# Kernel optimization log

Measured on AMD Instinct MI355X. Metric: run time of the kernel, lower is better.

The kernel has to match this reference:

```python
import jax, jax.numpy as jnp
import numpy as np

B, T, NH, HD = 2, 2048, 12, 128
HIDDEN = NH * HD
EPS = 1.1920928955078125e-07  # torch fp32 finfo eps (F.rms_norm default)


def _rope_cos_sin(T, d_half, base=10000.0):
    inv = 1.0 / (base ** (jnp.arange(d_half, dtype=jnp.float32) / d_half))
    t = jnp.arange(T, dtype=jnp.float32)
    f = t[:, None] * inv[None, :]  # [T, d_half]
    return jnp.cos(f)[None, :, None, :], jnp.sin(f)[None, :, None, :]


def apply_rotary_emb(x, cos, sin):
    d = x.shape[3] // 2
    x1, x2 = x[..., :d], x[..., d:]
    return jnp.concatenate([x1 * cos + x2 * sin, x1 * -sin + x2 * cos], axis=3)


def rms_norm(x):
    return x * jax.lax.rsqrt(jnp.mean(x * x, axis=-1, keepdims=True) + EPS)


def setup_inputs() -> dict:
    key = jax.random.key(0)
    ks = jax.random.split(key, 5)
    x = jax.random.normal(ks[0], (B, T, HIDDEN), dtype=jnp.float32)
    cos, sin = _rope_cos_sin(T, HD // 2)
    s = 1.0 / np.sqrt(HIDDEN)
    Wq = jax.random.normal(ks[1], (HIDDEN, HIDDEN), dtype=jnp.float32) * s
    Wk = jax.random.normal(ks[2], (HIDDEN, HIDDEN), dtype=jnp.float32) * s
    Wv = jax.random.normal(ks[3], (HIDDEN, HIDDEN), dtype=jnp.float32) * s
    Wp = jax.random.normal(ks[4], (HIDDEN, HIDDEN), dtype=jnp.float32) * s
    return {"x": x, "cos": cos, "sin": sin, "Wq": Wq, "Wk": Wk, "Wv": Wv,
            "Wp": Wp, "window": 1024}


def reference(x, cos, sin, Wq, Wk, Wv, Wp, window):
    Bx, Tx, _ = x.shape
    q = (x @ Wq.T).reshape(Bx, Tx, NH, HD)
    k = (x @ Wk.T).reshape(Bx, Tx, NH, HD)
    v = (x @ Wv.T).reshape(Bx, Tx, NH, HD)
    q = rms_norm(apply_rotary_emb(q, cos, sin))
    k = rms_norm(apply_rotary_emb(k, cos, sin))
    # causal + sliding-window attention (dense, matching the sdpa fallback)
    scale = 1.0 / np.sqrt(HD)
    scores = jnp.einsum('bqhd,bkhd->bhqk', q, k) * scale
    row = jnp.arange(Tx)[:, None]
    col = jnp.arange(Tx)[None, :]
    mask = (col <= row) & (row - col <= window)
    scores = jnp.where(mask[None, None], scores, jnp.finfo(scores.dtype).min)
    attn = jax.nn.softmax(scores, axis=-1)
    y = jnp.einsum('bhqk,bkhd->bqhd', attn, v).reshape(Bx, Tx, HIDDEN)
    return y @ Wp.T
```

## Files before the change

kernel.cpp:

```cpp
#include <hip/hip_runtime.h>
#include <stdint.h>

#define HIDDEN 1536
#define NHEAD 12
#define HD 128
#define TSEQ 2048
#define NROWS 4096
#define KDIM HIDDEN
#define EPS_F 1.1920928955078125e-07f
#define SCALE_LOG2E 0.12751879110195655f
#define FIXSUB 16.6f

typedef unsigned short u16;
typedef __bf16 bf16x8_t __attribute__((ext_vector_type(8)));
typedef float f32x4_t __attribute__((ext_vector_type(4)));

#define MFMA16(a, b, c) __builtin_amdgcn_mfma_f32_16x16x32_bf16((a), (b), (c), 0, 0, 0)
#define GLL(srcp, dstp) \
  __builtin_amdgcn_global_load_lds((const __attribute__((address_space(1))) void*)(srcp), \
                                   (__attribute__((address_space(3))) void*)(dstp), 16, 0, 0)

__device__ __forceinline__ u16 f2bf(float f) {
  unsigned u = __builtin_bit_cast(unsigned, f);
  u = (u + 0x7fffu + ((u >> 16) & 1u)) >> 16;
  return (u16)u;
}
__device__ __forceinline__ float bfu(u16 v) {
  return __builtin_bit_cast(float, ((unsigned)v) << 16);
}

__global__ __launch_bounds__(256) void cast_kernel(const float* __restrict__ in,
                                                   u16* __restrict__ out, int n) {
  int i = (blockIdx.x * 256 + threadIdx.x) * 4;
  if (i >= n) return;
  float4 v = *reinterpret_cast<const float4*>(in + i);
  uint2 pk;
  pk.x = (unsigned)f2bf(v.x) | ((unsigned)f2bf(v.y) << 16);
  pk.y = (unsigned)f2bf(v.z) | ((unsigned)f2bf(v.w) << 16);
  *reinterpret_cast<uint2*>(out + i) = pk;
}

__global__ __launch_bounds__(256) void cast4_kernel(
    const float* __restrict__ a, const float* __restrict__ b, const float* __restrict__ c,
    const float* __restrict__ d, u16* __restrict__ oa, u16* __restrict__ ob,
    u16* __restrict__ oc, u16* __restrict__ od, int n) {
  const float* in;
  u16* out;
  switch (blockIdx.y) {
    case 0: in = a; out = oa; break;
    case 1: in = b; out = ob; break;
    case 2: in = c; out = oc; break;
    default: in = d; out = od; break;
  }
  int i = (blockIdx.x * 256 + threadIdx.x) * 4;
  if (i >= n) return;
  float4 v = *reinterpret_cast<const float4*>(in + i);
  uint2 pk;
  pk.x = (unsigned)f2bf(v.x) | ((unsigned)f2bf(v.y) << 16);
  pk.y = (unsigned)f2bf(v.z) | ((unsigned)f2bf(v.w) << 16);
  *reinterpret_cast<uint2*>(out + i) = pk;
}

__device__ __forceinline__ void gemm_mainloop64(const u16* __restrict__ A,
                                                const u16* __restrict__ W, int M0, int N0,
                                                u16* lds, f32x4_t acc[4][4], int tid) {
  const int w = tid >> 6, l = tid & 63;
  const int lrow = l & 15, kg = l >> 4;
  const int wr = (w >> 1) * 64, wc = (w & 1) * 64;
  const int row0 = tid >> 3, j0 = tid & 7;
  const unsigned jsw = (unsigned)((j0 ^ (row0 & 7)) * 8);
  unsigned offA = (unsigned)((M0 + row0) * KDIM) + jsw;
  unsigned offW = (unsigned)((N0 + row0) * KDIM) + jsw;
  const u16* A1 = A + 32 * KDIM; const u16* A2 = A + 64 * KDIM; const u16* A3 = A + 96 * KDIM;
  const u16* W1 = W + 32 * KDIM; const u16* W2 = W + 64 * KDIM; const u16* W3 = W + 96 * KDIM;
  auto issue = [&](int buf) {
    u16* da = lds + buf * 8192 + w * 512;
    u16* dw = lds + 16384 + buf * 8192 + w * 512;
    GLL(A + offA, da);          GLL(A1 + offA, da + 2048);
    GLL(A2 + offA, da + 4096);  GLL(A3 + offA, da + 6144);
    GLL(W + offW, dw);          GLL(W1 + offW, dw + 2048);
    GLL(W2 + offW, dw + 4096);  GLL(W3 + offW, dw + 6144);
    offA += 64; offW += 64;
  };
  issue(0);
  const int NT = KDIM / 64;
#pragma unroll 1
  for (int kt = 0; kt < NT; ++kt) {
    const int cur = kt & 1;
    if (kt + 1 < NT) {
      issue(cur ^ 1);
      asm volatile("s_waitcnt vmcnt(8)" ::: "memory");
    } else {
      asm volatile("s_waitcnt vmcnt(0)" ::: "memory");
    }
    __builtin_amdgcn_s_barrier();
    asm volatile("" ::: "memory");
    const u16* Ab = lds + cur * 8192;
    const u16* Wb = lds + 16384 + cur * 8192;
#pragma unroll
    for (int s = 0; s < 2; ++s) {
      bf16x8_t af[4], bf_[4];
#pragma unroll
      for (int mi = 0; mi < 4; ++mi) {
        const int row = wr + mi * 16 + lrow;
        af[mi] = *reinterpret_cast<const bf16x8_t*>(Ab + row * 64 +
                                                    (((s << 2) | kg) ^ (row & 7)) * 8);
      }
#pragma unroll
      for (int ni = 0; ni < 4; ++ni) {
        const int row = wc + ni * 16 + lrow;
        bf_[ni] = *reinterpret_cast<const bf16x8_t*>(Wb + row * 64 +
                                                     (((s << 2) | kg) ^ (row & 7)) * 8);
      }
#pragma unroll
      for (int mi = 0; mi < 4; ++mi)
#pragma unroll
        for (int ni = 0; ni < 4; ++ni)
          acc[mi][ni] = MFMA16(af[mi], bf_[ni], acc[mi][ni]);
    }
    asm volatile("s_waitcnt lgkmcnt(0)" ::: "memory");
    __builtin_amdgcn_s_barrier();
    asm volatile("" ::: "memory");
  }
}

__global__ __launch_bounds__(256) void gemm_qkv_kernel(
    const u16* __restrict__ xb, const u16* __restrict__ wq, const u16* __restrict__ wk,
    const u16* __restrict__ wv, const float* __restrict__ cosp, const float* __restrict__ sinp,
    u16* __restrict__ qh, u16* __restrict__ kh, u16* __restrict__ vt) {
  __shared__ __align__(16) u16 lds[32768];
  const int tid = threadIdx.x;
  const int wgid = blockIdx.x;
  const int xcd = wgid & 7, c = wgid >> 3;
  const int m = ((xcd & 3) << 3) + (c & 7);
  const int nz = ((xcd >> 2) * 18) + (c >> 3);
  const int z = nz / 12, n = nz % 12;
  const int M0 = m * 128, N0 = n * 128;
  const u16* W = (z == 0) ? wq : (z == 1) ? wk : wv;
  f32x4_t acc[4][4] = {};
  gemm_mainloop64(xb, W, M0, N0, lds, acc, tid);
  const int w = tid >> 6, l = tid & 63;
  const int lrow = l & 15, kg = l >> 4;
  const int wr = (w >> 1) * 64, wc = (w & 1) * 64;
  char* cs = reinterpret_cast<char*>(lds);
  if (z == 2) {
#pragma unroll
    for (int mi = 0; mi < 4; ++mi)
#pragma unroll
      for (int ni = 0; ni < 4; ++ni)
#pragma unroll
        for (int r = 0; r < 4; ++r) {
          const int t_l = wr + mi * 16 + kg * 4 + r;
          const int d = wc + ni * 16 + lrow;
          const int bofs = (d * 256 + t_l * 2) ^ ((d & 7) << 4);
          *reinterpret_cast<u16*>(cs + bofs) = f2bf(acc[mi][ni][r]);
        }
  } else {
#pragma unroll
    for (int mi = 0; mi < 4; ++mi)
#pragma unroll
      for (int ni = 0; ni < 4; ++ni)
#pragma unroll
        for (int r = 0; r < 4; ++r) {
          const int t_l = wr + mi * 16 + kg * 4 + r;
          const int d = wc + ni * 16 + lrow;
          const int bofs = (t_l * 256 + d * 2) ^ ((t_l & 7) << 4);
          *reinterpret_cast<u16*>(cs + bofs) = f2bf(acc[mi][ni][r]);
        }
  }
  __syncthreads();
  const int rr = tid >> 1, hh = tid & 1;
  const int bb = M0 >> 11;
  const int t0 = M0 & (TSEQ - 1);
  const size_t bhn = (size_t)(bb * NHEAD + n);
  if (z == 2) {
    u16* dst = vt + (bhn * HD + rr) * TSEQ + t0 + hh * 64;
    const char* base = cs + rr * 256 + hh * 128;
#pragma unroll
    for (int j = 0; j < 8; ++j) {
      uint4 v = *reinterpret_cast<const uint4*>(base + ((j ^ (rr & 7)) * 16));
      *reinterpret_cast<uint4*>(dst + j * 8) = v;
    }
  } else {
    const int t = t0 + rr;
    const float* cosb = cosp + t * 64;
    const float* sinb = sinp + t * 64;
    const char* base = cs + rr * 256;
    float ss = 0.0f;
    unsigned pk[32];
#pragma unroll
    for (int j = 0; j < 8; ++j) {
      const int jp = (j ^ (rr & 7)) * 16;
      uint4 vo = *reinterpret_cast<const uint4*>(base + hh * 128 + jp);
      uint4 vx = *reinterpret_cast<const uint4*>(base + (hh ^ 1) * 128 + jp);
      const unsigned vo32[4] = {vo.x, vo.y, vo.z, vo.w};
      const unsigned vx32[4] = {vx.x, vx.y, vx.z, vx.w};
      const float* cj = cosb + j * 8;
      const float* sj = sinb + j * 8;
#pragma unroll
      for (int q2 = 0; q2 < 4; ++q2) {
        float o0 = bfu((u16)(vo32[q2] & 0xffffu)), o1 = bfu((u16)(vo32[q2] >> 16));
        float x0 = bfu((u16)(vx32[q2] & 0xffffu)), x1 = bfu((u16)(vx32[q2] >> 16));
        float cc0 = cj[q2 * 2], cc1 = cj[q2 * 2 + 1];
        float s0 = sj[q2 * 2], s1 = sj[q2 * 2 + 1];
        float y0 = hh ? __builtin_fmaf(o0, cc0, -x0 * s0) : __builtin_fmaf(o0, cc0, x0 * s0);
        float y1 = hh ? __builtin_fmaf(o1, cc1, -x1 * s1) : __builtin_fmaf(o1, cc1, x1 * s1);
        ss = __builtin_fmaf(y0, y0, __builtin_fmaf(y1, y1, ss));
        pk[j * 4 + q2] = (unsigned)f2bf(y0) | ((unsigned)f2bf(y1) << 16);
      }
    }
    ss += __shfl_xor(ss, 1, 64);
    const float rinv = rsqrtf(ss * (1.0f / 128.0f) + EPS_F);
    u16* dst = ((z == 0) ? qh : kh) + (bhn * TSEQ + t) * HD + hh * 64;
#pragma unroll
    for (int j = 0; j < 8; ++j) {
      unsigned o[4];
#pragma unroll
      for (int q2 = 0; q2 < 4; ++q2) {
        float y0 = bfu((u16)(pk[j * 4 + q2] & 0xffffu)) * rinv;
        float y1 = bfu((u16)(pk[j * 4 + q2] >> 16)) * rinv;
        o[q2] = (unsigned)f2bf(y0) | ((unsigned)f2bf(y1) << 16);
      }
      uint4 v;
      v.x = o[0]; v.y = o[1]; v.z = o[2]; v.w = o[3];
      *reinterpret_cast<uint4*>(dst + j * 8) = v;
    }
  }
}

__global__ __launch_bounds__(256) void gemm_out_kernel(const u16* __restrict__ yh,
                                                       const u16* __restrict__ wp,
                                                       float* __restrict__ out) {
  __shared__ __align__(16) u16 lds[32768];
  const int tid = threadIdx.x;
  const int wgid = blockIdx.x;
  const int xcd = wgid & 7, c = wgid >> 3;
  const int m = ((xcd & 3) << 3) + (c & 7);
  const int n = ((xcd >> 2) * 6) + (c >> 3);
  const int M0 = m * 128, N0 = n * 128;
  f32x4_t acc[4][4] = {};
  gemm_mainloop64(yh, wp, M0, N0, lds, acc, tid);
  const int w = tid >> 6, l = tid & 63;
  const int lrow = l & 15, kg = l >> 4;
  const int wr = (w >> 1) * 64, wc = (w & 1) * 64;
#pragma unroll
  for (int mi = 0; mi < 4; ++mi)
#pragma unroll
    for (int ni = 0; ni < 4; ++ni)
#pragma unroll
      for (int r = 0; r < 4; ++r) {
        const int grow = M0 + wr + mi * 16 + kg * 4 + r;
        const int gcol = N0 + wc + ni * 16 + lrow;
        out[(size_t)grow * HIDDEN + gcol] = acc[mi][ni][r];
      }
}

__global__ __launch_bounds__(512, 4) void attn_kernel(const u16* __restrict__ qh,
                                                      const u16* __restrict__ kh,
                                                      const u16* __restrict__ vt,
                                                      u16* __restrict__ yh,
                                                      const int* __restrict__ winp) {
  __shared__ __align__(16) u16 Kl[2][8192];
  __shared__ __align__(16) u16 Vl[8192];
  __shared__ __align__(16) u16 Pl[8][1024];
  const int tid = threadIdx.x, w = tid >> 6, l = tid & 63;
  const int lrow = l & 15, kg = l >> 4;
  const int bid = blockIdx.x;
  const int swz = (bid & 7) * 48 + (bid >> 3);
  const int qb = swz & 15;
  const int bh = swz >> 4;
  const int h = bh % NHEAD, b = bh / NHEAD;
  const int win = winp[0];
  const u16* Q = qh + (size_t)bh * TSEQ * HD;
  const u16* K = kh + (size_t)bh * TSEQ * HD;
  const u16* V = vt + (size_t)bh * HD * TSEQ;
  const int qw = qb * 128 + w * 16;
  bf16x8_t aq[4];
#pragma unroll
  for (int ks = 0; ks < 4; ++ks)
    aq[ks] = *reinterpret_cast<const bf16x8_t*>(Q + (qw + lrow) * HD + ks * 32 + kg * 8);
  float lrun[4] = {0.f, 0.f, 0.f, 0.f};
  f32x4_t accv[8] = {};
  int lo = qb * 128 - win;
  if (lo < 0) lo = 0;
  lo &= ~63;
  const int last = qb * 128 + 64;
  u16* Pw = &Pl[w][0];

  auto stage_k = [&](int kv, int buf) {
#pragma unroll
    for (int i = 0; i < 2; ++i) {
      const int c = i * 512 + w * 64 + l;
      const int row = c >> 4, j = c & 15;
      const u16* src = K + (size_t)(kv + row) * HD + ((j ^ (row & 7)) * 8);
      GLL(src, &Kl[buf][0] + i * 4096 + w * 512);
    }
  };
  auto stage_v = [&](int kv) {
#pragma unroll
    for (int i = 0; i < 2; ++i) {
      const int c = i * 512 + w * 64 + l;
      const int row = c >> 3, j = c & 7;
      const u16* src = V + (size_t)row * TSEQ + kv + ((j ^ (row & 7)) * 8);
      GLL(src, &Vl[0] + i * 4096 + w * 512);
    }
  };

  stage_k(lo, 0);
  int it = 0;
  for (int kv = lo; kv <= last; kv += 64, ++it) {
    const int cur = it & 1;
    stage_v(kv);
    stage_k(kv + 64, cur ^ 1);
    asm volatile("s_waitcnt vmcnt(4)" ::: "memory");
    __builtin_amdgcn_s_barrier();
    asm volatile("" ::: "memory");
    const u16* Kb = &Kl[cur][0];
    f32x4_t s[4] = {};
#pragma unroll
    for (int n = 0; n < 4; ++n) {
      const int row = n * 16 + lrow;
#pragma unroll
      for (int ks = 0; ks < 4; ++ks) {
        bf16x8_t bk = *reinterpret_cast<const bf16x8_t*>(
            Kb + row * 128 + (((ks << 2) | kg) ^ (row & 7)) * 8);
        s[n] = MFMA16(aq[ks], bk, s[n]);
      }
    }
    float ps[4][4];
    float psum[4];
#pragma unroll
    for (int n = 0; n < 4; ++n) {
      const int key = kv + n * 16 + lrow;
#pragma unroll
      for (int r = 0; r < 4; ++r) {
        const int rowq = qw + kg * 4 + r;
        const bool ok = (key <= rowq) && (rowq - key <= win);
        ps[n][r] = ok ? exp2f(__builtin_fmaf(s[n][r], SCALE_LOG2E, -FIXSUB)) : 0.0f;
      }
    }
#pragma unroll
    for (int r = 0; r < 4; ++r) psum[r] = (ps[0][r] + ps[1][r]) + (ps[2][r] + ps[3][r]);
#pragma unroll
    for (int off = 1; off < 16; off <<= 1)
#pragma unroll
      for (int r = 0; r < 4; ++r) psum[r] += __shfl_xor(psum[r], off, 64);
#pragma unroll
    for (int r = 0; r < 4; ++r) lrun[r] += psum[r];
#pragma unroll
    for (int n = 0; n < 4; ++n)
#pragma unroll
      for (int r = 0; r < 4; ++r) {
        const int rp = kg * 4 + r;
        int bofs = rp * 128 + (n * 16 + lrow) * 2;
        bofs ^= (rp & 7) << 4;
        *reinterpret_cast<u16*>(reinterpret_cast<char*>(Pw) + bofs) = f2bf(ps[n][r]);
      }
    asm volatile("s_waitcnt lgkmcnt(0)" ::: "memory");
    asm volatile("s_waitcnt vmcnt(2)" ::: "memory");
    __builtin_amdgcn_s_barrier();
    asm volatile("" ::: "memory");
    bf16x8_t ap[2];
#pragma unroll
    for (int k2 = 0; k2 < 2; ++k2) {
      int bofs = lrow * 128 + k2 * 64 + kg * 16;
      bofs ^= (lrow & 7) << 4;
      ap[k2] = *reinterpret_cast<const bf16x8_t*>(reinterpret_cast<const char*>(Pw) + bofs);
    }
#pragma unroll
    for (int k2 = 0; k2 < 2; ++k2)
#pragma unroll
      for (int dn = 0; dn < 8; ++dn) {
        const int row = dn * 16 + lrow;
        bf16x8_t bv = *reinterpret_cast<const bf16x8_t*>(
            Vl + row * 64 + (((k2 << 2) | kg) ^ (row & 7)) * 8);
        accv[dn] = MFMA16(ap[k2], bv, accv[dn]);
      }
    __builtin_amdgcn_s_barrier();
    asm volatile("" ::: "memory");
  }
  float inv[4];
#pragma unroll
  for (int r = 0; r < 4; ++r) inv[r] = 1.0f / lrun[r];
#pragma unroll
  for (int dn = 0; dn < 8; ++dn)
#pragma unroll
    for (int r = 0; r < 4; ++r) {
      const int rowg = b * TSEQ + qw + kg * 4 + r;
      const int col = h * HD + dn * 16 + lrow;
      yh[(size_t)rowg * HIDDEN + col] = f2bf(accv[dn][r] * inv[r]);
    }
}

extern "C" void kernel_launch(void* const* d_in, const int* in_sizes, int n_in, void* d_out,
                              int out_size, void* d_ws, size_t ws_size, hipStream_t stream) {
  const float* x = (const float*)d_in[0];
  const float* cosp = (const float*)d_in[1];
  const float* sinp = (const float*)d_in[2];
  const float* Wq = (const float*)d_in[3];
  const float* Wk = (const float*)d_in[4];
  const float* Wv = (const float*)d_in[5];
  const float* Wp = (const float*)d_in[6];
  const int* winp = (const int*)d_in[7];

  char* ws = (char*)d_ws;
  size_t off = 0;
  auto alloc = [&](size_t bytes) {
    char* p = ws + off;
    off += (bytes + 255) & ~(size_t)255;
    return p;
  };
  u16* xb = (u16*)alloc((size_t)NROWS * HIDDEN * 2);
  u16* wqb = (u16*)alloc((size_t)HIDDEN * HIDDEN * 2);
  u16* wkb = (u16*)alloc((size_t)HIDDEN * HIDDEN * 2);
  u16* wvb = (u16*)alloc((size_t)HIDDEN * HIDDEN * 2);
  u16* wpb = (u16*)alloc((size_t)HIDDEN * HIDDEN * 2);
  u16* qh = (u16*)alloc((size_t)NROWS * HIDDEN * 2);
  u16* kh = (u16*)alloc((size_t)NROWS * HIDDEN * 2);
  u16* vt = (u16*)alloc((size_t)NROWS * HIDDEN * 2);
  u16* yh = (u16*)alloc((size_t)NROWS * HIDDEN * 2);

  const int nx = NROWS * HIDDEN;
  const int nw = HIDDEN * HIDDEN;
  cast_kernel<<<nx / 1024, 256, 0, stream>>>(x, xb, nx);
  cast4_kernel<<<dim3(nw / 1024, 4), 256, 0, stream>>>(Wq, Wk, Wv, Wp, wqb, wkb, wvb, wpb, nw);

  gemm_qkv_kernel<<<dim3(1152), 256, 0, stream>>>(xb, wqb, wkb, wvb, cosp, sinp, qh, kh, vt);
  attn_kernel<<<dim3(384), 512, 0, stream>>>(qh, kh, vt, yh, winp);
  gemm_out_kernel<<<dim3(384), 256, 0, stream>>>(yh, wpb, (float*)d_out);
}
```

Before: 196.8 us.

## Double-buffer V tiles, skip masking on interior blocks, defer row-sum reduction

Gives V its own double buffer so the next K and V tiles are prefetched a full iteration ahead, which removes the end-of-iteration barrier and one vmcnt wait. Blocks that lie fully inside the causal and sliding window now skip the per-element mask test. The cross-lane shuffle reduction of the softmax row sum moves out of the loop to a single pass at the end. In exchange, shared memory grows by 16 KB per block, which may lower occupancy. The last iteration re-prefetches the final tile redundantly.

New measurement: 185.9 us (median of 3 runs). 1.06x faster.

```diff
diff --git a/kernel.cpp b/kernel.cpp
--- a/kernel.cpp
+++ b/kernel.cpp
@@ -261,7 +261,7 @@
                                                       u16* __restrict__ yh,
                                                       const int* __restrict__ winp) {
   __shared__ __align__(16) u16 Kl[2][8192];
-  __shared__ __align__(16) u16 Vl[8192];
+  __shared__ __align__(16) u16 Vl[2][8192];
   __shared__ __align__(16) u16 Pl[8][1024];
   const int tid = threadIdx.x, w = tid >> 6, l = tid & 63;
   const int lrow = l & 15, kg = l >> 4;
@@ -279,12 +279,13 @@
 #pragma unroll
   for (int ks = 0; ks < 4; ++ks)
     aq[ks] = *reinterpret_cast<const bf16x8_t*>(Q + (qw + lrow) * HD + ks * 32 + kg * 8);
-  float lrun[4] = {0.f, 0.f, 0.f, 0.f};
+  float lsum[4] = {0.f, 0.f, 0.f, 0.f};
   f32x4_t accv[8] = {};
   int lo = qb * 128 - win;
   if (lo < 0) lo = 0;
   lo &= ~63;
   const int last = qb * 128 + 64;
+
   u16* Pw = &Pl[w][0];
 
   auto stage_k = [&](int kv, int buf) {
@@ -296,25 +297,27 @@
       GLL(src, &Kl[buf][0] + i * 4096 + w * 512);
     }
   };
-  auto stage_v = [&](int kv) {
+  auto stage_v = [&](int kv, int buf) {
 #pragma unroll
     for (int i = 0; i < 2; ++i) {
       const int c = i * 512 + w * 64 + l;
       const int row = c >> 3, j = c & 7;
       const u16* src = V + (size_t)row * TSEQ + kv + ((j ^ (row & 7)) * 8);
-      GLL(src, &Vl[0] + i * 4096 + w * 512);
+      GLL(src, &Vl[buf][0] + i * 4096 + w * 512);
     }
   };
 
   stage_k(lo, 0);
+  stage_v(lo, 0);
   int it = 0;
   for (int kv = lo; kv <= last; kv += 64, ++it) {
     const int cur = it & 1;
-    stage_v(kv);
-    stage_k(kv + 64, cur ^ 1);
-    asm volatile("s_waitcnt vmcnt(4)" ::: "memory");
+    const int kpre = (kv + 64 <= last) ? kv + 64 : last;
+    stage_k(kpre, cur ^ 1);
+    asm volatile("s_waitcnt vmcnt(2)" ::: "memory");
     __builtin_amdgcn_s_barrier();
     asm volatile("" ::: "memory");
+    stage_v(kpre, cur ^ 1);
     const u16* Kb = &Kl[cur][0];
     f32x4_t s[4] = {};
 #pragma unroll
@@ -328,25 +331,28 @@
       }
     }
     float ps[4][4];
-    float psum[4];
-#pragma unroll
-    for (int n = 0; n < 4; ++n) {
-      const int key = kv + n * 16 + lrow;
-#pragma unroll
-      for (int r = 0; r < 4; ++r) {
-        const int rowq = qw + kg * 4 + r;
-        const bool ok = (key <= rowq) && (rowq - key <= win);
-        ps[n][r] = ok ? exp2f(__builtin_fmaf(s[n][r], SCALE_LOG2E, -FIXSUB)) : 0.0f;
-      }
-    }
-#pragma unroll
-    for (int r = 0; r < 4; ++r) psum[r] = (ps[0][r] + ps[1][r]) + (ps[2][r] + ps[3][r]);
-#pragma unroll
-    for (int off = 1; off < 16; off <<= 1)
-#pragma unroll
-      for (int r = 0; r < 4; ++r) psum[r] += __shfl_xor(psum[r], off, 64);
-#pragma unroll
-    for (int r = 0; r < 4; ++r) lrun[r] += psum[r];
+    const bool interior = (kv + 63 <= qw) && ((qw + 15) - kv <= win);
+    if (interior) {
+#pragma unroll
+      for (int n = 0; n < 4; ++n)
+#pragma unroll
+        for (int r = 0; r < 4; ++r)
+          ps[n][r] = exp2f(__builtin_fmaf(s[n][r], SCALE_LOG2E, -FIXSUB));
+    } else {
+#pragma unroll
+      for (int n = 0; n < 4; ++n) {
+        const int key = kv + n * 16 + lrow;
+#pragma unroll
+        for (int r = 0; r < 4; ++r) {
+          const int rowq = qw + kg * 4 + r;
+          const bool ok = (key <= rowq) && (rowq - key <= win);
+          ps[n][r] = ok ? exp2f(__builtin_fmaf(s[n][r], SCALE_LOG2E, -FIXSUB)) : 0.0f;
+        }
+      }
+    }
+#pragma unroll
+    for (int r = 0; r < 4; ++r)
+      lsum[r] += (ps[0][r] + ps[1][r]) + (ps[2][r] + ps[3][r]);
 #pragma unroll
     for (int n = 0; n < 4; ++n)
 #pragma unroll
@@ -357,7 +363,6 @@
         *reinterpret_cast<u16*>(reinterpret_cast<char*>(Pw) + bofs) = f2bf(ps[n][r]);
       }
     asm volatile("s_waitcnt lgkmcnt(0)" ::: "memory");
-    asm volatile("s_waitcnt vmcnt(2)" ::: "memory");
     __builtin_amdgcn_s_barrier();
     asm volatile("" ::: "memory");
     bf16x8_t ap[2];
@@ -367,21 +372,24 @@
       bofs ^= (lrow & 7) << 4;
       ap[k2] = *reinterpret_cast<const bf16x8_t*>(reinterpret_cast<const char*>(Pw) + bofs);
     }
+    const u16* Vb = &Vl[cur][0];
 #pragma unroll
     for (int k2 = 0; k2 < 2; ++k2)
 #pragma unroll
       for (int dn = 0; dn < 8; ++dn) {
         const int row = dn * 16 + lrow;
         bf16x8_t bv = *reinterpret_cast<const bf16x8_t*>(
-            Vl + row * 64 + (((k2 << 2) | kg) ^ (row & 7)) * 8);
+            Vb + row * 64 + (((k2 << 2) | kg) ^ (row & 7)) * 8);
         accv[dn] = MFMA16(ap[k2], bv, accv[dn]);
       }
-    __builtin_amdgcn_s_barrier();
-    asm volatile("" ::: "memory");
   }
+#pragma unroll
+  for (int off = 1; off < 16; off <<= 1)
+#pragma unroll
+    for (int r = 0; r < 4; ++r) lsum[r] += __shfl_xor(lsum[r], off, 64);
   float inv[4];
 #pragma unroll
-  for (int r = 0; r < 4; ++r) inv[r] = 1.0f / lrun[r];
+  for (int r = 0; r < 4; ++r) inv[r] = 1.0f / lsum[r];
 #pragma unroll
   for (int dn = 0; dn < 8; ++dn)
 #pragma unroll
```
